# Performance work log

Hardware: AMD Instinct MI355X
Metric: run time of the kernel (lower is better)

The kernel has to match this reference:

```python
import jax, jax.numpy as jnp
import numpy as np

GX, GY, GZ = 128, 128, 16   # voxel_range
N = 100000                  # occupied voxels
C = 64                      # channels (inc == outc)
K = 27                      # 3x3x3 kernel offsets
EPS = 1e-5
NEG_SLOPE = 0.01            # LeakyReLU default


def _kernel_map():
    """Build sparse-conv neighbor map: nbr[k, n] = row index of the input voxel at
    coord[n] + offset[k], or N (sentinel -> zero feature) if unoccupied/out of range."""
    rng = np.random.RandomState(0)
    flat = rng.choice(GX * GY * GZ, size=N, replace=False)
    x = flat // (GY * GZ)
    rem = flat % (GY * GZ)
    y = rem // GZ
    z = rem % GZ
    lut = np.full(GX * GY * GZ, N, dtype=np.int32)
    lut[flat] = np.arange(N, dtype=np.int32)
    offs = [(i, j, k) for i in (-1, 0, 1) for j in (-1, 0, 1) for k in (-1, 0, 1)]
    nbr = np.full((K, N), N, dtype=np.int32)
    for ki, (dx, dy, dz) in enumerate(offs):
        xs, ys, zs = x + dx, y + dy, z + dz
        valid = (xs >= 0) & (xs < GX) & (ys >= 0) & (ys < GY) & (zs >= 0) & (zs < GZ)
        fl = (np.clip(xs, 0, GX - 1) * (GY * GZ)
              + np.clip(ys, 0, GY - 1) * GZ
              + np.clip(zs, 0, GZ - 1))
        nbr[ki] = np.where(valid, lut[fl], N)
    return jnp.asarray(nbr)


def setup_inputs() -> dict:
    key = jax.random.key(0)
    k0, k1, k2 = jax.random.split(key, 3)
    w_scale = 1.0 / np.sqrt(C * K)  # Minkowski-style fan-in init
    return {
        "feats": jax.random.normal(k0, (N, C), jnp.float32),
        "W1": jax.random.normal(k1, (K, C, C), jnp.float32) * w_scale,
        "g1": jnp.ones((C,), jnp.float32),
        "b1": jnp.zeros((C,), jnp.float32),
        "W2": jax.random.normal(k2, (K, C, C), jnp.float32) * w_scale,
        "g2": jnp.ones((C,), jnp.float32),
        "b2": jnp.zeros((C,), jnp.float32),
        "nbr_idx": _kernel_map(),
    }


def _sparse_conv(f, W, nbr):
    # gather-GEMM-scatter: fp has a zero sentinel row at index N
    fp = jnp.concatenate([f, jnp.zeros((1, f.shape[1]), f.dtype)], axis=0)
    g = fp[nbr]                                # [K, N, Cin] gathered neighbors
    return jnp.einsum('knc,kco->no', g, W)     # [N, Cout]


def _bn(x, gamma, beta):
    # training-mode BatchNorm over all active voxels, per channel
    m = jnp.mean(x, axis=0)
    v = jnp.var(x, axis=0)
    return (x - m) * jax.lax.rsqrt(v + EPS) * gamma + beta


def _lrelu(x):
    return jnp.where(x >= 0, x, NEG_SLOPE * x)


def reference(feats, W1, g1, b1, W2, g2, b2, nbr_idx):
    skip = feats  # downsample is identity (inc == outc, stride == 1)
    y = _lrelu(_bn(_sparse_conv(feats, W1, nbr_idx), g1, b1))
    y = _lrelu(_bn(_sparse_conv(y, W2, nbr_idx), g2, b2))
    return _lrelu(skip + y)
```

## Files before the change

### kernel.cpp

```cpp
#include <hip/hip_runtime.h>
#include <hip/hip_bf16.h>


#define N_VOX 100000
#define NCH 64
#define NK 27
#define ROWS 128
#define NBLK ((N_VOX + ROWS - 1) / ROWS)

typedef __hip_bfloat16 bf16;
typedef __attribute__((ext_vector_type(8))) short bf16x8;
typedef __attribute__((ext_vector_type(4))) float f32x4;

__device__ __forceinline__ float b2f(short s) {
  unsigned u = ((unsigned)(unsigned short)s) << 16;
  return __builtin_bit_cast(float, u);
}
__device__ __forceinline__ short f2b(float f) {
  __hip_bfloat16 h = __float2bfloat16(f);
  return __builtin_bit_cast(short, h);
}

__device__ __forceinline__ void gload16(const void* g, void* l) {
  __builtin_amdgcn_global_load_lds(
      (const __attribute__((address_space(1))) void*)g,
      (__attribute__((address_space(3))) void*)l, 16, 0, 0);
}

__global__ void cast_feats(const float* __restrict__ feats, bf16* __restrict__ fbf) {
  const size_t i = ((size_t)blockIdx.x * 256 + threadIdx.x) * 8;
  if (i >= (size_t)(N_VOX + 1) * NCH) return;
  bf16x8 o;
  if (i < (size_t)N_VOX * NCH) {
    const f32x4 v0 = *reinterpret_cast<const f32x4*>(feats + i);
    const f32x4 v1 = *reinterpret_cast<const f32x4*>(feats + i + 4);
#pragma unroll
    for (int e = 0; e < 8; ++e) o[e] = f2b(e < 4 ? v0[e] : v1[e - 4]);
  } else {
#pragma unroll
    for (int e = 0; e < 8; ++e) o[e] = 0;
  }
  *reinterpret_cast<bf16x8*>((short*)fbf + i) = o;
}

__global__ void pack_w(const float* __restrict__ W1, const float* __restrict__ W2,
                       bf16* __restrict__ wp1, bf16* __restrict__ wp2) {
  const int t = blockIdx.x * 256 + threadIdx.x;
  const int half = NK * 4 * 2 * 64;
  if (t >= 2 * half) return;
  const float* W = (t < half) ? W1 : W2;
  short* wp = (short*)((t < half) ? wp1 : wp2);
  const int q = (t < half) ? t : t - half;
  const int l  = q & 63;
  const int kb = (q >> 6) & 1;
  const int j  = (q >> 7) & 3;
  const int k  = q >> 9;
  const int oo = j * 16 + (l & 15);
  const int c0 = kb * 32 + (l >> 4) * 8;
  bf16x8 v;
#pragma unroll
  for (int e = 0; e < 8; ++e)
    v[e] = f2b(W[((size_t)k * 64 + c0 + e) * 64 + oo]);
  *reinterpret_cast<bf16x8*>(&wp[(size_t)q * 8]) = v;
}

__global__ __launch_bounds__(256, 4)
void conv_mfma(const bf16* __restrict__ feat, const bf16* __restrict__ wp,
               const int* __restrict__ nbr, bf16* __restrict__ y,
               float* __restrict__ part) {
  __shared__ short GB[3][8 * 512];
  __shared__ int nbrL[NK * ROWS];
  __shared__ float redS[4][NCH];
  __shared__ float redQ[4][NCH];

  const int tid = threadIdx.x;
  const int lane = tid & 63;
  const int wv = tid >> 6;

  const int nwg = NBLK;
  const int xcd = blockIdx.x & 7;
  const int pos = blockIdx.x >> 3;
  const int q8 = nwg >> 3, r8 = nwg & 7;
  const int bid = (xcd < r8 ? xcd * (q8 + 1) : r8 * (q8 + 1) + (xcd - r8) * q8) + pos;
  const int n0 = bid * ROWS;

  for (int t = tid; t < NK * ROWS; t += 256) {
    const int k = t >> 7;
    const int rr = t & (ROWS - 1);
    nbrL[t] = (n0 + rr < N_VOX) ? nbr[(size_t)k * N_VOX + n0 + rr] : N_VOX;
  }
  __syncthreads();

  const int r0 = wv * 32 + (lane & 15);
  const int koff = (lane >> 4) * 8;

  f32x4 acc[2][4];
#pragma unroll
  for (int h = 0; h < 2; ++h)
#pragma unroll
    for (int j = 0; j < 4; ++j)
      acc[h][j] = (f32x4){0.f, 0.f, 0.f, 0.f};

  bf16x8 AE[4], AO[4];

#define LOAD_A(A, k)                                                        \
  {                                                                         \
    const int i0 = nbrL[(k) * ROWS + r0];                                   \
    const int i1 = nbrL[(k) * ROWS + r0 + 16];                              \
    A[0] = *reinterpret_cast<const bf16x8*>(feat + (size_t)i0 * 64 + koff); \
    A[1] = *reinterpret_cast<const bf16x8*>(feat + (size_t)i0 * 64 + 32 + koff); \
    A[2] = *reinterpret_cast<const bf16x8*>(feat + (size_t)i1 * 64 + koff); \
    A[3] = *reinterpret_cast<const bf16x8*>(feat + (size_t)i1 * 64 + 32 + koff); \
  }

#define STAGE_B(slot, k)                                                    \
  {                                                                         \
    const short* srcb = (const short*)wp + (size_t)(k) * 4096 +             \
                        (wv * 2) * 512 + lane * 8;                          \
    gload16((const void*)srcb, (void*)&GB[slot][(wv * 2) * 512]);           \
    gload16((const void*)(srcb + 512), (void*)&GB[slot][(wv * 2 + 1) * 512]); \
  }

#define MFMA_TAP(A, B)                                                      \
  _Pragma("unroll")                                                         \
  for (int h = 0; h < 2; ++h)                                               \
    _Pragma("unroll")                                                       \
    for (int j = 0; j < 4; ++j)                                             \
      _Pragma("unroll")                                                     \
      for (int kb = 0; kb < 2; ++kb)                                        \
        acc[h][j] = __builtin_amdgcn_mfma_f32_16x16x32_bf16(                \
            A[h * 2 + kb], B[j * 2 + kb], acc[h][j], 0, 0, 0);

#define TILE_STEP(Acur, Aoth, t, cur)                                       \
  {                                                                         \
    asm volatile("s_waitcnt vmcnt(2)" ::: "memory");                        \
    __builtin_amdgcn_sched_barrier(0);                                      \
    __builtin_amdgcn_s_barrier();                                           \
    LOAD_A(Aoth, (t) + 1)                                                   \
    if ((t) <= NK - 3) {                                                    \
      const int stslot = (cur) >= 1 ? (cur) - 1 : 2;           \
      STAGE_B(stslot, (t) + 2)                                              \
    }                                                                       \
    __builtin_amdgcn_sched_barrier(0);       \
    bf16x8 Bf[8];                                                           \
    _Pragma("unroll")                                                       \
    for (int f = 0; f < 8; ++f)                                             \
      Bf[f] = *reinterpret_cast<const bf16x8*>(&GB[cur][f * 512 + lane * 8]); \
    MFMA_TAP(Acur, Bf)                                                      \
  }

  STAGE_B(0, 0)
  LOAD_A(AE, 0)
  STAGE_B(1, 1)

  int cur = 0;
#pragma unroll 1
  for (int j = 0; j < 13; ++j) {
    const int t = 2 * j;
    TILE_STEP(AE, AO, t, cur)
    cur = (cur == 2) ? 0 : cur + 1;
    TILE_STEP(AO, AE, t + 1, cur)
    cur = (cur == 2) ? 0 : cur + 1;
  }
  {
    asm volatile("s_waitcnt vmcnt(0)" ::: "memory");
    __builtin_amdgcn_sched_barrier(0);
    __builtin_amdgcn_s_barrier();
    bf16x8 Bf[8];
#pragma unroll
    for (int f = 0; f < 8; ++f)
      Bf[f] = *reinterpret_cast<const bf16x8*>(&GB[2][f * 512 + lane * 8]);
    MFMA_TAP(AE, Bf)
  }

#undef LOAD_A
#undef STAGE_B
#undef MFMA_TAP
#undef TILE_STEP

#pragma unroll
  for (int h = 0; h < 2; ++h)
#pragma unroll
    for (int j = 0; j < 4; ++j) {
      const int col = j * 16 + (lane & 15);
#pragma unroll
      for (int r = 0; r < 4; ++r) {
        const int row = n0 + wv * 32 + h * 16 + (lane >> 4) * 4 + r;
        if (row < N_VOX) ((short*)y)[(size_t)row * NCH + col] = f2b(acc[h][j][r]);
      }
    }

#pragma unroll
  for (int j = 0; j < 4; ++j) {
    float s1 = 0.f, s2 = 0.f;
#pragma unroll
    for (int h = 0; h < 2; ++h)
#pragma unroll
      for (int r = 0; r < 4; ++r) {
        const float v = acc[h][j][r];
        s1 += v;
        s2 += v * v;
      }
    s1 += __shfl_xor(s1, 16); s2 += __shfl_xor(s2, 16);
    s1 += __shfl_xor(s1, 32); s2 += __shfl_xor(s2, 32);
    if (lane < 16) {
      redS[wv][j * 16 + lane] = s1;
      redQ[wv][j * 16 + lane] = s2;
    }
  }
  __syncthreads();
  if (tid < NCH) {
    const float s1 = redS[0][tid] + redS[1][tid] + redS[2][tid] + redS[3][tid];
    const float s2 = redQ[0][tid] + redQ[1][tid] + redQ[2][tid] + redQ[3][tid];
    part[(size_t)blockIdx.x * 128 + tid] = s1;
    part[(size_t)blockIdx.x * 128 + 64 + tid] = s2;
  }
}

__global__ void finalize(const float* __restrict__ part, int nblk,
                         const float* __restrict__ g, const float* __restrict__ b,
                         float* __restrict__ ab) {
  __shared__ float r1[256], r2[256];
  const int c = blockIdx.x;
  const int t = threadIdx.x;
  float s1 = 0.f, s2 = 0.f;
  for (int bb = t; bb < nblk; bb += 256) {
    s1 += part[(size_t)bb * 128 + c];
    s2 += part[(size_t)bb * 128 + 64 + c];
  }
  r1[t] = s1; r2[t] = s2;
  __syncthreads();
  for (int off = 128; off > 0; off >>= 1) {
    if (t < off) { r1[t] += r1[t + off]; r2[t] += r2[t + off]; }
    __syncthreads();
  }
  if (t == 0) {
    const float m = r1[0] / (float)N_VOX;
    const float v = r2[0] / (float)N_VOX - m * m;
    const float a = g[c] * rsqrtf(v + 1e-5f);
    const float sh = b[c] - m * a;
    ab[c] = a;
    ab[64 + c] = sh;
  }
}

__global__ void bn_act(const bf16* __restrict__ y, const float* __restrict__ ab,
                       bf16* __restrict__ z) {
  const size_t i = ((size_t)blockIdx.x * 256 + threadIdx.x) * 8;
  if (i >= (size_t)(N_VOX + 1) * NCH) return;
  const int col = (int)(i & 63);
  bf16x8 o;
  if (i < (size_t)N_VOX * NCH) {
    const bf16x8 v = *reinterpret_cast<const bf16x8*>((const short*)y + i);
#pragma unroll
    for (int e = 0; e < 8; ++e) {
      float x = b2f(v[e]) * ab[col + e] + ab[64 + col + e];
      x = x < 0.f ? 0.01f * x : x;
      o[e] = f2b(x);
    }
  } else {
#pragma unroll
    for (int e = 0; e < 8; ++e) o[e] = 0;
  }
  *reinterpret_cast<bf16x8*>((short*)z + i) = o;
}

__global__ void bn_act_res(const bf16* __restrict__ y, const float* __restrict__ ab,
                           const float* __restrict__ feats, float* __restrict__ out) {
  const size_t i = ((size_t)blockIdx.x * 256 + threadIdx.x) * 8;
  const int col = (int)(i & 63);
  const bf16x8 v = *reinterpret_cast<const bf16x8*>((const short*)y + i);
  const f32x4 s0 = *reinterpret_cast<const f32x4*>(feats + i);
  const f32x4 s1 = *reinterpret_cast<const f32x4*>(feats + i + 4);
  f32x4 o0, o1;
#pragma unroll
  for (int e = 0; e < 8; ++e) {
    float x = b2f(v[e]) * ab[col + e] + ab[64 + col + e];
    x = x < 0.f ? 0.01f * x : x;
    float r = (e < 4 ? s0[e] : s1[e - 4]) + x;
    r = r < 0.f ? 0.01f * r : r;
    if (e < 4) o0[e] = r; else o1[e - 4] = r;
  }
  *reinterpret_cast<f32x4*>(out + i) = o0;
  *reinterpret_cast<f32x4*>(out + i + 4) = o1;
}

extern "C" void kernel_launch(void* const* d_in, const int* in_sizes, int n_in,
                              void* d_out, int out_size, void* d_ws, size_t ws_size,
                              hipStream_t stream) {
  const float* feats = (const float*)d_in[0];
  const float* W1 = (const float*)d_in[1];
  const float* g1 = (const float*)d_in[2];
  const float* b1 = (const float*)d_in[3];
  const float* W2 = (const float*)d_in[4];
  const float* g2 = (const float*)d_in[5];
  const float* b2 = (const float*)d_in[6];
  const int* nbr = (const int*)d_in[7];
  float* out = (float*)d_out;

  char* p = (char*)d_ws;
  bf16* fbf = (bf16*)p; p += (size_t)(N_VOX + 1) * NCH * 2;
  bf16* ybf = (bf16*)p; p += (size_t)N_VOX * NCH * 2;
  bf16* z = (bf16*)p;   p += (size_t)(N_VOX + 1) * NCH * 2;
  bf16* wp1 = (bf16*)p; p += 442368;
  bf16* wp2 = (bf16*)p; p += 442368;
  float* part = (float*)p; p += (size_t)NBLK * 128 * 4;
  float* ab1 = (float*)p; p += 512;
  float* ab2 = (float*)p; p += 512;

  const int cast_blocks = (int)(((size_t)(N_VOX + 1) * NCH / 8 + 255) / 256);

  cast_feats<<<cast_blocks, 256, 0, stream>>>(feats, fbf);
  pack_w<<<108, 256, 0, stream>>>(W1, W2, wp1, wp2);

  conv_mfma<<<NBLK, 256, 0, stream>>>(fbf, wp1, nbr, ybf, part);
  finalize<<<64, 256, 0, stream>>>(part, NBLK, g1, b1, ab1);
  bn_act<<<cast_blocks, 256, 0, stream>>>(ybf, ab1, z);

  conv_mfma<<<NBLK, 256, 0, stream>>>(z, wp2, nbr, ybf, part);
  finalize<<<64, 256, 0, stream>>>(part, NBLK, g2, b2, ab2);
  bn_act_res<<<(N_VOX * NCH / 8) / 256, 256, 0, stream>>>(ybf, ab2, feats, out);
}
```

Before: 134.7 us.

## Process two kernel taps per barrier epoch with four-slot weight ring

Restructures the gather-GEMM main loop so each barrier epoch computes two taps while prefetching the A rows and B weights for the next two taps. The weight LDS ring grows from three to four slots and the A register buffers double. The aim is to halve the number of barriers and waits and to keep more gathers in flight. In exchange it waits on vmcnt(0) each epoch, raises register and LDS use, and lowers the occupancy target from 4 to 3 blocks per CU.

```diff
diff --git a/kernel.cpp b/kernel.cpp
--- a/kernel.cpp
+++ b/kernel.cpp
@@ -64,11 +64,11 @@
   *reinterpret_cast<bf16x8*>(&wp[(size_t)q * 8]) = v;
 }
 
-__global__ __launch_bounds__(256, 4)
+__global__ __launch_bounds__(256, 3)
 void conv_mfma(const bf16* __restrict__ feat, const bf16* __restrict__ wp,
                const int* __restrict__ nbr, bf16* __restrict__ y,
                float* __restrict__ part) {
-  __shared__ short GB[3][8 * 512];
+  __shared__ short GB[4][8 * 512];
   __shared__ int nbrL[NK * ROWS];
   __shared__ float redS[4][NCH];
   __shared__ float redQ[4][NCH];
@@ -101,7 +101,7 @@
     for (int j = 0; j < 4; ++j)
       acc[h][j] = (f32x4){0.f, 0.f, 0.f, 0.f};
 
-  bf16x8 AE[4], AO[4];
+  bf16x8 AE0[4], AE1[4], AO0[4], AO1[4];
 
 #define LOAD_A(A, k)                                                        \
   {                                                                         \
@@ -131,52 +131,63 @@
         acc[h][j] = __builtin_amdgcn_mfma_f32_16x16x32_bf16(                \
             A[h * 2 + kb], B[j * 2 + kb], acc[h][j], 0, 0, 0);
 
-#define TILE_STEP(Acur, Aoth, t, cur)                                       \
+#define EPOCH(Ac0, Ac1, An0, An1, t)                                        \
   {                                                                         \
-    asm volatile("s_waitcnt vmcnt(2)" ::: "memory");                        \
+    asm volatile("s_waitcnt vmcnt(0)" ::: "memory");                        \
     __builtin_amdgcn_sched_barrier(0);                                      \
     __builtin_amdgcn_s_barrier();                                           \
-    LOAD_A(Aoth, (t) + 1)                                                   \
-    if ((t) <= NK - 3) {                                                    \
-      const int stslot = (cur) >= 1 ? (cur) - 1 : 2;           \
-      STAGE_B(stslot, (t) + 2)                                              \
+    __builtin_amdgcn_sched_barrier(0);                                      \
+    LOAD_A(An0, (t) + 2)                                                    \
+    if ((t) + 3 < NK) LOAD_A(An1, (t) + 3)                                  \
+    STAGE_B(((t) + 2) & 3, (t) + 2)                                         \
+    if ((t) + 3 < NK) STAGE_B(((t) + 3) & 3, (t) + 3)                       \
+    __builtin_amdgcn_sched_barrier(0);                                      \
+    {                                                                       \
+      bf16x8 Bf0[8];                                                        \
+      _Pragma("unroll")                                                     \
+      for (int f = 0; f < 8; ++f)                                           \
+        Bf0[f] = *reinterpret_cast<const bf16x8*>(                          \
+            &GB[(t) & 3][f * 512 + lane * 8]);                              \
+      MFMA_TAP(Ac0, Bf0)                                                    \
     }                                                                       \
-    __builtin_amdgcn_sched_barrier(0);       \
-    bf16x8 Bf[8];                                                           \
-    _Pragma("unroll")                                                       \
-    for (int f = 0; f < 8; ++f)                                             \
-      Bf[f] = *reinterpret_cast<const bf16x8*>(&GB[cur][f * 512 + lane * 8]); \
-    MFMA_TAP(Acur, Bf)                                                      \
+    {                                                                       \
+      bf16x8 Bf1[8];                                                        \
+      _Pragma("unroll")                                                     \
+      for (int f = 0; f < 8; ++f)                                           \
+        Bf1[f] = *reinterpret_cast<const bf16x8*>(                          \
+            &GB[((t) + 1) & 3][f * 512 + lane * 8]);                        \
+      MFMA_TAP(Ac1, Bf1)                                                    \
+    }                                                                       \
   }
 
   STAGE_B(0, 0)
-  LOAD_A(AE, 0)
   STAGE_B(1, 1)
-
-  int cur = 0;
+  LOAD_A(AE0, 0)
+  LOAD_A(AE1, 1)
+
 #pragma unroll 1
-  for (int j = 0; j < 13; ++j) {
-    const int t = 2 * j;
-    TILE_STEP(AE, AO, t, cur)
-    cur = (cur == 2) ? 0 : cur + 1;
-    TILE_STEP(AO, AE, t + 1, cur)
-    cur = (cur == 2) ? 0 : cur + 1;
-  }
+  for (int j = 0; j < 6; ++j) {
+    const int t = 4 * j;
+    EPOCH(AE0, AE1, AO0, AO1, t)
+    EPOCH(AO0, AO1, AE0, AE1, t + 2)
+  }
+  EPOCH(AE0, AE1, AO0, AO1, 24)
   {
     asm volatile("s_waitcnt vmcnt(0)" ::: "memory");
     __builtin_amdgcn_sched_barrier(0);
     __builtin_amdgcn_s_barrier();
+    __builtin_amdgcn_sched_barrier(0);
     bf16x8 Bf[8];
 #pragma unroll
     for (int f = 0; f < 8; ++f)
       Bf[f] = *reinterpret_cast<const bf16x8*>(&GB[2][f * 512 + lane * 8]);
-    MFMA_TAP(AE, Bf)
+    MFMA_TAP(AO0, Bf)
   }
 
 #undef LOAD_A
 #undef STAGE_B
 #undef MFMA_TAP
-#undef TILE_STEP
+#undef EPOCH
 
 #pragma unroll
   for (int h = 0; h < 2; ++h)
```

After: 150.4 us. 1.12x slower.

## Deepen gather/weight prefetch pipeline to two taps ahead with four LDS slots

Applied to the files above, without the earlier changes.

The MFMA sparse-conv loop now prefetches the gathered A fragments and the staged weight tiles two kernel taps ahead instead of one. It uses three rotating A register sets and a four-slot LDS ring for B, with the loop restructured into a 3-way unrolled body and a peeled tail. The intent is to hide more of the irregular neighbor-gather latency behind the MFMAs. In exchange it needs more registers and LDS, so launch bounds drop from 4 to 3 blocks per CU, which reduces occupancy.

```diff
diff --git a/kernel.cpp b/kernel.cpp
--- a/kernel.cpp
+++ b/kernel.cpp
@@ -64,11 +64,11 @@
   *reinterpret_cast<bf16x8*>(&wp[(size_t)q * 8]) = v;
 }
 
-__global__ __launch_bounds__(256, 4)
+__global__ __launch_bounds__(256, 3)
 void conv_mfma(const bf16* __restrict__ feat, const bf16* __restrict__ wp,
                const int* __restrict__ nbr, bf16* __restrict__ y,
                float* __restrict__ part) {
-  __shared__ short GB[3][8 * 512];
+  __shared__ short GB[4][8 * 512];
   __shared__ int nbrL[NK * ROWS];
   __shared__ float redS[4][NCH];
   __shared__ float redQ[4][NCH];
@@ -101,7 +101,7 @@
     for (int j = 0; j < 4; ++j)
       acc[h][j] = (f32x4){0.f, 0.f, 0.f, 0.f};
 
-  bf16x8 AE[4], AO[4];
+  bf16x8 A0[4], A1[4], A2[4];
 
 #define LOAD_A(A, k)                                                        \
   {                                                                         \
@@ -131,52 +131,63 @@
         acc[h][j] = __builtin_amdgcn_mfma_f32_16x16x32_bf16(                \
             A[h * 2 + kb], B[j * 2 + kb], acc[h][j], 0, 0, 0);
 
-#define TILE_STEP(Acur, Aoth, t, cur)                                       \
+#define TILE(Acur, Aload, t)                                                \
   {                                                                         \
-    asm volatile("s_waitcnt vmcnt(2)" ::: "memory");                        \
+    asm volatile("s_waitcnt vmcnt(6)" ::: "memory");                        \
     __builtin_amdgcn_sched_barrier(0);                                      \
     __builtin_amdgcn_s_barrier();                                           \
-    LOAD_A(Aoth, (t) + 1)                                                   \
-    if ((t) <= NK - 3) {                                                    \
-      const int stslot = (cur) >= 1 ? (cur) - 1 : 2;           \
-      STAGE_B(stslot, (t) + 2)                                              \
-    }                                                                       \
-    __builtin_amdgcn_sched_barrier(0);       \
+    __builtin_amdgcn_sched_barrier(0);                                      \
+    LOAD_A(Aload, (t) + 2)                                                  \
+    STAGE_B(((t) + 2) & 3, (t) + 2)                                         \
+    __builtin_amdgcn_sched_barrier(0);                                      \
     bf16x8 Bf[8];                                                           \
     _Pragma("unroll")                                                       \
     for (int f = 0; f < 8; ++f)                                             \
-      Bf[f] = *reinterpret_cast<const bf16x8*>(&GB[cur][f * 512 + lane * 8]); \
+      Bf[f] = *reinterpret_cast<const bf16x8*>(                             \
+          &GB[(t) & 3][f * 512 + lane * 8]);                                \
     MFMA_TAP(Acur, Bf)                                                      \
   }
 
   STAGE_B(0, 0)
-  LOAD_A(AE, 0)
+  LOAD_A(A0, 0)
   STAGE_B(1, 1)
-
-  int cur = 0;
+  LOAD_A(A1, 1)
+
 #pragma unroll 1
-  for (int j = 0; j < 13; ++j) {
-    const int t = 2 * j;
-    TILE_STEP(AE, AO, t, cur)
-    cur = (cur == 2) ? 0 : cur + 1;
-    TILE_STEP(AO, AE, t + 1, cur)
-    cur = (cur == 2) ? 0 : cur + 1;
+  for (int i = 0; i < 8; ++i) {
+    const int t = 3 * i;
+    TILE(A0, A2, t)
+    TILE(A1, A0, t + 1)
+    TILE(A2, A1, t + 2)
+  }
+  TILE(A0, A2, 24)
+  {
+    asm volatile("s_waitcnt vmcnt(6)" ::: "memory");
+    __builtin_amdgcn_sched_barrier(0);
+    __builtin_amdgcn_s_barrier();
+    __builtin_amdgcn_sched_barrier(0);
+    bf16x8 Bf[8];
+#pragma unroll
+    for (int f = 0; f < 8; ++f)
+      Bf[f] = *reinterpret_cast<const bf16x8*>(&GB[1][f * 512 + lane * 8]);
+    MFMA_TAP(A1, Bf)
   }
   {
     asm volatile("s_waitcnt vmcnt(0)" ::: "memory");
     __builtin_amdgcn_sched_barrier(0);
     __builtin_amdgcn_s_barrier();
+    __builtin_amdgcn_sched_barrier(0);
     bf16x8 Bf[8];
 #pragma unroll
     for (int f = 0; f < 8; ++f)
       Bf[f] = *reinterpret_cast<const bf16x8*>(&GB[2][f * 512 + lane * 8]);
-    MFMA_TAP(AE, Bf)
+    MFMA_TAP(A2, Bf)
   }
 
 #undef LOAD_A
 #undef STAGE_B
 #undef MFMA_TAP
-#undef TILE_STEP
+#undef TILE
 
 #pragma unroll
   for (int h = 0; h < 2; ++h)
```

Result: slower. 158.9 us (+17.9%).

## Split conv kernel taps across two workgroups per row block, reduce in separate pass

Applied to the files above, without the earlier changes.

Each 128-row block of the sparse conv is now handled by two workgroups, one covering taps 0-13 and the other 13-26, so twice as many workgroups are launched to raise occupancy and parallelism across CUs. Each half writes a bf16 partial result, and a new sum_bn kernel adds the two halves while computing the BatchNorm partial sums that were previously fused into the conv epilogue. This adds an extra full-tensor write and read per conv, an extra launch, and a second bf16 rounding of the partial sums, in exchange for shorter per-workgroup dependency chains. Launch bounds change from 4 to 3 waves per SIMD.

```diff
diff --git a/kernel.cpp b/kernel.cpp
--- a/kernel.cpp
+++ b/kernel.cpp
@@ -64,30 +64,33 @@
   *reinterpret_cast<bf16x8*>(&wp[(size_t)q * 8]) = v;
 }
 
-__global__ __launch_bounds__(256, 4)
+__global__ __launch_bounds__(256, 3)
 void conv_mfma(const bf16* __restrict__ feat, const bf16* __restrict__ wp,
-               const int* __restrict__ nbr, bf16* __restrict__ y,
-               float* __restrict__ part) {
-  __shared__ short GB[3][8 * 512];
-  __shared__ int nbrL[NK * ROWS];
-  __shared__ float redS[4][NCH];
-  __shared__ float redQ[4][NCH];
+               const int* __restrict__ nbr, bf16* __restrict__ y0,
+               bf16* __restrict__ y1) {
+  __shared__ short GB[3][4096];
+  __shared__ int nbrL[14 * ROWS];
 
   const int tid = threadIdx.x;
   const int lane = tid & 63;
   const int wv = tid >> 6;
 
-  const int nwg = NBLK;
+  const int nwg = 2 * NBLK;
   const int xcd = blockIdx.x & 7;
   const int pos = blockIdx.x >> 3;
   const int q8 = nwg >> 3, r8 = nwg & 7;
   const int bid = (xcd < r8 ? xcd * (q8 + 1) : r8 * (q8 + 1) + (xcd - r8) * q8) + pos;
-  const int n0 = bid * ROWS;
-
-  for (int t = tid; t < NK * ROWS; t += 256) {
+  const int rb = bid >> 1;
+  const int khalf = bid & 1;
+  const int n0 = rb * ROWS;
+  const int k0 = khalf ? 14 : 0;
+  const int NT = khalf ? 13 : 14;
+  bf16* y = khalf ? y1 : y0;
+
+  for (int t = tid; t < NT * ROWS; t += 256) {
     const int k = t >> 7;
     const int rr = t & (ROWS - 1);
-    nbrL[t] = (n0 + rr < N_VOX) ? nbr[(size_t)k * N_VOX + n0 + rr] : N_VOX;
+    nbrL[t] = (n0 + rr < N_VOX) ? nbr[(size_t)(k0 + k) * N_VOX + n0 + rr] : N_VOX;
   }
   __syncthreads();
 
@@ -103,19 +106,19 @@
 
   bf16x8 AE[4], AO[4];
 
-#define LOAD_A(A, k)                                                        \
+#define LOAD_A(A, t)                                                        \
   {                                                                         \
-    const int i0 = nbrL[(k) * ROWS + r0];                                   \
-    const int i1 = nbrL[(k) * ROWS + r0 + 16];                              \
+    const int i0 = nbrL[(t) * ROWS + r0];                                   \
+    const int i1 = nbrL[(t) * ROWS + r0 + 16];                              \
     A[0] = *reinterpret_cast<const bf16x8*>(feat + (size_t)i0 * 64 + koff); \
     A[1] = *reinterpret_cast<const bf16x8*>(feat + (size_t)i0 * 64 + 32 + koff); \
     A[2] = *reinterpret_cast<const bf16x8*>(feat + (size_t)i1 * 64 + koff); \
     A[3] = *reinterpret_cast<const bf16x8*>(feat + (size_t)i1 * 64 + 32 + koff); \
   }
 
-#define STAGE_B(slot, k)                                                    \
+#define STAGE_B(slot, t)                                                    \
   {                                                                         \
-    const short* srcb = (const short*)wp + (size_t)(k) * 4096 +             \
+    const short* srcb = (const short*)wp + (size_t)(k0 + (t)) * 4096 +      \
                         (wv * 2) * 512 + lane * 8;                          \
     gload16((const void*)srcb, (void*)&GB[slot][(wv * 2) * 512]);           \
     gload16((const void*)(srcb + 512), (void*)&GB[slot][(wv * 2 + 1) * 512]); \
@@ -131,21 +134,21 @@
         acc[h][j] = __builtin_amdgcn_mfma_f32_16x16x32_bf16(                \
             A[h * 2 + kb], B[j * 2 + kb], acc[h][j], 0, 0, 0);
 
-#define TILE_STEP(Acur, Aoth, t, cur)                                       \
+#define TILE(Acur, Aoth, t)                                                 \
   {                                                                         \
-    asm volatile("s_waitcnt vmcnt(2)" ::: "memory");                        \
+    if ((t) < NT - 1) { asm volatile("s_waitcnt vmcnt(2)" ::: "memory"); }  \
+    else              { asm volatile("s_waitcnt vmcnt(0)" ::: "memory"); }  \
     __builtin_amdgcn_sched_barrier(0);                                      \
     __builtin_amdgcn_s_barrier();                                           \
-    LOAD_A(Aoth, (t) + 1)                                                   \
-    if ((t) <= NK - 3) {                                                    \
-      const int stslot = (cur) >= 1 ? (cur) - 1 : 2;           \
-      STAGE_B(stslot, (t) + 2)                                              \
-    }                                                                       \
-    __builtin_amdgcn_sched_barrier(0);       \
+    if ((t) + 1 < NT) LOAD_A(Aoth, (t) + 1)                                 \
+    if ((t) + 2 < NT) { STAGE_B(((t) + 2) % 3, (t) + 2) }                   \
+    __builtin_amdgcn_sched_barrier(0);                                      \
     bf16x8 Bf[8];                                                           \
+    const int rdslot = (t) % 3;                                             \
     _Pragma("unroll")                                                       \
     for (int f = 0; f < 8; ++f)                                             \
-      Bf[f] = *reinterpret_cast<const bf16x8*>(&GB[cur][f * 512 + lane * 8]); \
+      Bf[f] = *reinterpret_cast<const bf16x8*>(                             \
+          &GB[rdslot][f * 512 + lane * 8]);                                 \
     MFMA_TAP(Acur, Bf)                                                      \
   }
 
@@ -153,30 +156,17 @@
   LOAD_A(AE, 0)
   STAGE_B(1, 1)
 
-  int cur = 0;
 #pragma unroll 1
-  for (int j = 0; j < 13; ++j) {
-    const int t = 2 * j;
-    TILE_STEP(AE, AO, t, cur)
-    cur = (cur == 2) ? 0 : cur + 1;
-    TILE_STEP(AO, AE, t + 1, cur)
-    cur = (cur == 2) ? 0 : cur + 1;
-  }
-  {
-    asm volatile("s_waitcnt vmcnt(0)" ::: "memory");
-    __builtin_amdgcn_sched_barrier(0);
-    __builtin_amdgcn_s_barrier();
-    bf16x8 Bf[8];
-#pragma unroll
-    for (int f = 0; f < 8; ++f)
-      Bf[f] = *reinterpret_cast<const bf16x8*>(&GB[2][f * 512 + lane * 8]);
-    MFMA_TAP(AE, Bf)
-  }
+  for (int t = 0; t + 1 < NT; t += 2) {
+    TILE(AE, AO, t)
+    TILE(AO, AE, t + 1)
+  }
+  if (NT & 1) { TILE(AE, AO, NT - 1) }
 
 #undef LOAD_A
 #undef STAGE_B
 #undef MFMA_TAP
-#undef TILE_STEP
+#undef TILE
 
 #pragma unroll
   for (int h = 0; h < 2; ++h)
@@ -189,31 +179,46 @@
         if (row < N_VOX) ((short*)y)[(size_t)row * NCH + col] = f2b(acc[h][j][r]);
       }
     }
-
-#pragma unroll
-  for (int j = 0; j < 4; ++j) {
-    float s1 = 0.f, s2 = 0.f;
-#pragma unroll
-    for (int h = 0; h < 2; ++h)
-#pragma unroll
-      for (int r = 0; r < 4; ++r) {
-        const float v = acc[h][j][r];
-        s1 += v;
-        s2 += v * v;
-      }
-    s1 += __shfl_xor(s1, 16); s2 += __shfl_xor(s2, 16);
-    s1 += __shfl_xor(s1, 32); s2 += __shfl_xor(s2, 32);
-    if (lane < 16) {
-      redS[wv][j * 16 + lane] = s1;
-      redQ[wv][j * 16 + lane] = s2;
+}
+
+__global__ void sum_bn(bf16* __restrict__ y0, const bf16* __restrict__ y1,
+                       float* __restrict__ part) {
+  __shared__ float red[4][128];
+  const int tid = threadIdx.x;
+  const int lane = tid & 63;
+  const int wv = tid >> 6;
+  const size_t i = ((size_t)blockIdx.x * 256 + tid) * 8;
+
+  const bf16x8 a = *reinterpret_cast<const bf16x8*>((const short*)y0 + i);
+  const bf16x8 b = *reinterpret_cast<const bf16x8*>((const short*)y1 + i);
+  bf16x8 o;
+  float s1[8], s2[8];
+#pragma unroll
+  for (int e = 0; e < 8; ++e) {
+    const float v = b2f(a[e]) + b2f(b[e]);
+    o[e] = f2b(v);
+    s1[e] = v;
+    s2[e] = v * v;
+  }
+  *reinterpret_cast<bf16x8*>((short*)y0 + i) = o;
+
+#pragma unroll
+  for (int e = 0; e < 8; ++e) {
+    s1[e] += __shfl_down(s1[e], 8);  s2[e] += __shfl_down(s2[e], 8);
+    s1[e] += __shfl_down(s1[e], 16); s2[e] += __shfl_down(s2[e], 16);
+    s1[e] += __shfl_down(s1[e], 32); s2[e] += __shfl_down(s2[e], 32);
+  }
+  if (lane < 8) {
+#pragma unroll
+    for (int e = 0; e < 8; ++e) {
+      red[wv][lane * 8 + e] = s1[e];
+      red[wv][64 + lane * 8 + e] = s2[e];
     }
   }
   __syncthreads();
-  if (tid < NCH) {
-    const float s1 = redS[0][tid] + redS[1][tid] + redS[2][tid] + redS[3][tid];
-    const float s2 = redQ[0][tid] + redQ[1][tid] + redQ[2][tid] + redQ[3][tid];
-    part[(size_t)blockIdx.x * 128 + tid] = s1;
-    part[(size_t)blockIdx.x * 128 + 64 + tid] = s2;
+  if (tid < 128) {
+    part[(size_t)blockIdx.x * 128 + tid] =
+        red[0][tid] + red[1][tid] + red[2][tid] + red[3][tid];
   }
 }
 
@@ -300,24 +305,28 @@
 
   char* p = (char*)d_ws;
   bf16* fbf = (bf16*)p; p += (size_t)(N_VOX + 1) * NCH * 2;
-  bf16* ybf = (bf16*)p; p += (size_t)N_VOX * NCH * 2;
+  bf16* yh0 = (bf16*)p; p += (size_t)N_VOX * NCH * 2;
+  bf16* yh1 = (bf16*)p; p += (size_t)N_VOX * NCH * 2;
   bf16* z = (bf16*)p;   p += (size_t)(N_VOX + 1) * NCH * 2;
   bf16* wp1 = (bf16*)p; p += 442368;
   bf16* wp2 = (bf16*)p; p += 442368;
-  float* part = (float*)p; p += (size_t)NBLK * 128 * 4;
+  float* part = (float*)p; p += (size_t)3125 * 128 * 4;
   float* ab1 = (float*)p; p += 512;
   float* ab2 = (float*)p; p += 512;
 
   const int cast_blocks = (int)(((size_t)(N_VOX + 1) * NCH / 8 + 255) / 256);
+  const int sum_blocks = (int)((size_t)N_VOX * NCH / 8 / 256);
 
   cast_feats<<<cast_blocks, 256, 0, stream>>>(feats, fbf);
   pack_w<<<108, 256, 0, stream>>>(W1, W2, wp1, wp2);
 
-  conv_mfma<<<NBLK, 256, 0, stream>>>(fbf, wp1, nbr, ybf, part);
-  finalize<<<64, 256, 0, stream>>>(part, NBLK, g1, b1, ab1);
-  bn_act<<<cast_blocks, 256, 0, stream>>>(ybf, ab1, z);
-
-  conv_mfma<<<NBLK, 256, 0, stream>>>(z, wp2, nbr, ybf, part);
-  finalize<<<64, 256, 0, stream>>>(part, NBLK, g2, b2, ab2);
-  bn_act_res<<<(N_VOX * NCH / 8) / 256, 256, 0, stream>>>(ybf, ab2, feats, out);
-}
+  conv_mfma<<<2 * NBLK, 256, 0, stream>>>(fbf, wp1, nbr, yh0, yh1);
+  sum_bn<<<sum_blocks, 256, 0, stream>>>(yh0, yh1, part);
+  finalize<<<64, 256, 0, stream>>>(part, sum_blocks, g1, b1, ab1);
+  bn_act<<<cast_blocks, 256, 0, stream>>>(yh0, ab1, z);
+
+  conv_mfma<<<2 * NBLK, 256, 0, stream>>>(z, wp2, nbr, yh0, yh1);
+  sum_bn<<<sum_blocks, 256, 0, stream>>>(yh0, yh1, part);
+  finalize<<<64, 256, 0, stream>>>(part, sum_blocks, g2, b2, ab2);
+  bn_act_res<<<sum_blocks, 256, 0, stream>>>(yh0, ab2, feats, out);
+}
```

After: 156.5 us. 16.2% more time.
